# Optimization experiments

Hardware: AMD Instinct MI355X
Metric: run time of the kernel (lower is better)

## Reference

```python
import jax, jax.numpy as jnp
import numpy as np
from jax import lax

V, B, C_IN, T = 8, 32, 8, 4096
O, K, H = 64, 5, 16  # out_channels, kernel, SE hidden (O // reduction)
PAD = (K - 1) // 2


def setup_inputs() -> dict:
    key = jax.random.key(0)
    ks = jax.random.split(key, 8)
    return {
        "x": jax.random.normal(ks[0], (V, B, C_IN, T), dtype=jnp.float32),
        "conv_w": jax.random.uniform(ks[1], (O, 1, K), dtype=jnp.float32),
        "conv_b": jax.random.uniform(ks[2], (O,), dtype=jnp.float32),
        "se_w1": jax.random.normal(ks[3], (V, H, O), dtype=jnp.float32) * 0.1,
        "se_b1": jax.random.normal(ks[4], (V, H), dtype=jnp.float32) * 0.1,
        "se_w2": jax.random.normal(ks[5], (V, O, H), dtype=jnp.float32) * 0.1,
        "se_b2": jax.random.normal(ks[6], (V, O), dtype=jnp.float32) * 0.1,
        "attn_w": jax.random.normal(ks[7], (2 * O,), dtype=jnp.float32) * 0.1,
    }


def reference(x, conv_w, conv_b, se_w1, se_b1, se_w2, se_b2, attn_w):
    # _CommonConv1d: per-out-channel depthwise conv summed over input channels
    # == conv1d(sum over input channels) with weight [O,1,K].
    xs = x.sum(axis=2).reshape(V * B, 1, T)  # [V*B, 1, T]
    conv = lax.conv_general_dilated(
        xs, conv_w, window_strides=(1,), padding=[(PAD, PAD)],
        dimension_numbers=("NCH", "OIH", "NCH"))  # [V*B, O, T]
    conv = conv + conv_b[None, :, None]
    conv = jax.nn.selu(conv).reshape(V, B, O, T)  # conv_outputs, SELU activation

    # Per-vertex squeeze-excitation gating, then AdaptiveAvgPool1d(1)
    s = conv.mean(axis=-1)  # [V, B, O]
    h = jax.nn.relu(jnp.einsum("vbo,vho->vbh", s, se_w1) + se_b1[:, None, :])
    gate = jax.nn.sigmoid(jnp.einsum("vbh,voh->vbo", h, se_w2) + se_b2[:, None, :])
    compressed = (conv * gate[..., None]).mean(axis=-1)  # [V, B, O]

    # Pairwise self-attention over all (v_from, v_to) pairs
    cf = jnp.broadcast_to(compressed[:, None], (V, V, B, O))   # v_from
    ct = jnp.broadcast_to(compressed[None, :], (V, V, B, O))   # v_to
    feat = jnp.concatenate([cf, ct], axis=-1)                  # [Vf, Vt, B, 2O]
    aw = jax.nn.selu(jnp.einsum("fgbc,c->fgb", feat, attn_w))  # [Vf, Vt, B]
    sm = jax.nn.softmax(aw, axis=0)                            # softmax over v_from

    # outputs[v_to] = sum_f sm[f, v_to] * conv_outputs[f]
    out = jnp.einsum("fgb,fbot->gbot", sm, conv)  # [Vt, B, O, T]
    return out
```

## Files before the change

### kernel.cpp

```cpp
#include <hip/hip_runtime.h>

#define V 8
#define B 32
#define CIN 8
#define T 4096
#define O 64
#define K 5
#define H 16

#define XSTRIDE 4104

#define XS_OFF 0
#define S_OFF  (V*B*XSTRIDE)
#define AF_OFF (S_OFF + V*B*O)
#define AT_OFF (AF_OFF + V*B)
#define SM_OFF (AT_OFF + V*B)

__device__ __forceinline__ float selu_f(float x) {
    const float SC = 1.0507009873554805f;
    const float SA = 1.7580993408473766f;
    float e = __expf(x);
    float neg = SA * e - SA;
    return x > 0.0f ? SC * x : neg;
}

__global__ void k_xs(const float* __restrict__ x, float* __restrict__ ws) {
    int row = blockIdx.x;
    int tid = threadIdx.x;
    const float* xr = x + (size_t)row * CIN * T;
    float* xp = ws + XS_OFF + (size_t)row * XSTRIDE;
    for (int t = tid; t < T; t += 256) {
        float a = 0.0f;
        #pragma unroll
        for (int c = 0; c < CIN; ++c) a += xr[c * T + t];
        xp[t + 4] = a;
    }
    if (tid < 4) { xp[tid] = 0.0f; xp[4100 + tid] = 0.0f; }
}

__global__ void k_mean(const float* __restrict__ ws, const float* __restrict__ cw,
                       const float* __restrict__ cb, float* __restrict__ s_out) {
    int row = blockIdx.x;
    int tid = threadIdx.x;
    int wave = tid >> 6;
    int lane = tid & 63;
    const float* xp = ws + XS_OFF + (size_t)row * XSTRIDE;
    float w0 = cw[lane * 5 + 0], w1 = cw[lane * 5 + 1], w2 = cw[lane * 5 + 2];
    float w3 = cw[lane * 5 + 3], w4 = cw[lane * 5 + 4];
    float bv = cb[lane];
    int c0 = wave * 512;
    float a0 = xp[c0 + 2], a1 = xp[c0 + 3], a2 = xp[c0 + 4], a3 = xp[c0 + 5];
    float acc = 0.0f;
    #pragma unroll 8
    for (int t = c0; t < c0 + 512; ++t) {
        float a4 = xp[t + 6];
        float cv = bv + w0 * a0 + w1 * a1 + w2 * a2 + w3 * a3 + w4 * a4;
        acc += selu_f(cv);
        a0 = a1; a1 = a2; a2 = a3; a3 = a4;
    }
    __shared__ float part[8][64];
    part[wave][lane] = acc;
    __syncthreads();
    if (tid < 64) {
        float tot = 0.0f;
        #pragma unroll
        for (int w = 0; w < 8; ++w) tot += part[w][tid];
        s_out[row * 64 + tid] = tot * (1.0f / (float)T);
    }
}

__global__ void k_se(const float* __restrict__ s_in, const float* __restrict__ w1,
                     const float* __restrict__ b1, const float* __restrict__ w2,
                     const float* __restrict__ b2, const float* __restrict__ awv,
                     float* __restrict__ af, float* __restrict__ at) {
    int blk = blockIdx.x;
    int v = blk >> 5;
    int b = blk & 31;
    int o = threadIdx.x;
    __shared__ float ssh[64];
    __shared__ float hsh[16];
    float so = s_in[blk * 64 + o];
    ssh[o] = so;
    __syncthreads();
    if (o < 16) {
        float hv = b1[v * 16 + o];
        #pragma unroll
        for (int j = 0; j < 64; ++j) hv += ssh[j] * w1[(v * 16 + o) * 64 + j];
        hsh[o] = fmaxf(hv, 0.0f);
    }
    __syncthreads();
    float gv = b2[v * 64 + o];
    #pragma unroll
    for (int j = 0; j < 16; ++j) gv += hsh[j] * w2[(v * 64 + o) * 16 + j];
    float gate = 1.0f / (1.0f + __expf(-gv));
    float comp = so * gate;
    float pf = comp * awv[o];
    float pt = comp * awv[64 + o];
    #pragma unroll
    for (int m = 32; m >= 1; m >>= 1) {
        pf += __shfl_xor(pf, m, 64);
        pt += __shfl_xor(pt, m, 64);
    }
    if (o == 0) { af[v * 32 + b] = pf; at[v * 32 + b] = pt; }
}

__global__ void k_sm(const float* __restrict__ af, const float* __restrict__ at,
                     float* __restrict__ sm) {
    int b = blockIdx.x;
    int tid = threadIdx.x;
    int f = tid >> 3, g = tid & 7;
    float a = selu_f(af[f * 32 + b] + at[g * 32 + b]);
    float m = a;
    m = fmaxf(m, __shfl_xor(m, 8, 64));
    m = fmaxf(m, __shfl_xor(m, 16, 64));
    m = fmaxf(m, __shfl_xor(m, 32, 64));
    float e = __expf(a - m);
    float ssum = e;
    ssum += __shfl_xor(ssum, 8, 64);
    ssum += __shfl_xor(ssum, 16, 64);
    ssum += __shfl_xor(ssum, 32, 64);
    sm[b * 64 + tid] = e / ssum;
}

__global__ void k_out(const float* __restrict__ ws, const float* __restrict__ cw,
                      const float* __restrict__ cb, float* __restrict__ out) {
    int blk = blockIdx.x;
    int b = blk >> 6;
    int r = blk & 63;
    int tile = r >> 2;
    int og = r & 3;
    int t = tile * 256 + threadIdx.x;

    const float* smp = ws + SM_OFF + b * 64;
    float smv[64];
    #pragma unroll
    for (int i = 0; i < 64; ++i) smv[i] = smp[i];

    float xw[8][5];
    #pragma unroll
    for (int f = 0; f < 8; ++f) {
        const float* xp = ws + XS_OFF + (size_t)(f * B + b) * XSTRIDE + t + 2;
        #pragma unroll
        for (int j = 0; j < 5; ++j) xw[f][j] = xp[j];
    }

    #pragma unroll 1
    for (int oi = 0; oi < 16; ++oi) {
        int o = og * 16 + oi;
        float w0 = cw[o * 5 + 0], w1 = cw[o * 5 + 1], w2 = cw[o * 5 + 2];
        float w3 = cw[o * 5 + 3], w4 = cw[o * 5 + 4];
        float bv = cb[o];
        float cf[8];
        #pragma unroll
        for (int f = 0; f < 8; ++f) {
            float cv = bv + w0 * xw[f][0] + w1 * xw[f][1] + w2 * xw[f][2]
                          + w3 * xw[f][3] + w4 * xw[f][4];
            cf[f] = selu_f(cv);
        }
        #pragma unroll
        for (int g = 0; g < 8; ++g) {
            float acc = 0.0f;
            #pragma unroll
            for (int f = 0; f < 8; ++f) acc += smv[f * 8 + g] * cf[f];
            out[((size_t)(g * B + b) * O + o) * T + t] = acc;
        }
    }
}

extern "C" void kernel_launch(void* const* d_in, const int* in_sizes, int n_in,
                              void* d_out, int out_size, void* d_ws, size_t ws_size,
                              hipStream_t stream) {
    const float* x      = (const float*)d_in[0];
    const float* conv_w = (const float*)d_in[1];
    const float* conv_b = (const float*)d_in[2];
    const float* se_w1  = (const float*)d_in[3];
    const float* se_b1  = (const float*)d_in[4];
    const float* se_w2  = (const float*)d_in[5];
    const float* se_b2  = (const float*)d_in[6];
    const float* attn_w = (const float*)d_in[7];
    float* out = (float*)d_out;
    float* ws  = (float*)d_ws;

    k_xs<<<V * B, 256, 0, stream>>>(x, ws);
    k_mean<<<V * B, 512, 0, stream>>>(ws, conv_w, conv_b, ws + S_OFF);
    k_se<<<V * B, 64, 0, stream>>>(ws + S_OFF, se_w1, se_b1, se_w2, se_b2, attn_w,
                                   ws + AF_OFF, ws + AT_OFF);
    k_sm<<<B, 64, 0, stream>>>(ws + AF_OFF, ws + AT_OFF, ws + SM_OFF);
    k_out<<<B * (T / 256) * 4, 256, 0, stream>>>(ws, conv_w, conv_b, out);
}
```

Before: 113.0 us.

## Fuse prep kernels and vectorize output kernel with 4 timesteps per thread

Fuses the channel-sum kernel with the conv/SELU mean kernel, keeping the summed row in shared memory, and fuses the SE gating with the softmax kernel, which cuts five launches to three. The output kernel now computes four consecutive timesteps per thread from an 8-wide register window, writes float4 stores, and loads weights and softmax values through readfirstlane so they become uniform scalar values. The aim is less launch overhead, less global traffic and wider memory transactions. In exchange the output grid shrinks to 512 blocks, and the larger per-thread accumulator set raises register pressure and may reduce occupancy.

```diff
diff --git a/kernel.cpp b/kernel.cpp
--- a/kernel.cpp
+++ b/kernel.cpp
@@ -12,9 +12,7 @@
 
 #define XS_OFF 0
 #define S_OFF  (V*B*XSTRIDE)
-#define AF_OFF (S_OFF + V*B*O)
-#define AT_OFF (AF_OFF + V*B)
-#define SM_OFF (AT_OFF + V*B)
+#define SM_OFF (S_OFF + V*B*O)
 
 __device__ __forceinline__ float selu_f(float x) {
     const float SC = 1.0507009873554805f;
@@ -24,36 +22,53 @@
     return x > 0.0f ? SC * x : neg;
 }
 
-__global__ void k_xs(const float* __restrict__ x, float* __restrict__ ws) {
+__device__ __forceinline__ float sload(const float* p) {
+    return __int_as_float(__builtin_amdgcn_readfirstlane(__float_as_int(*p)));
+}
+
+__global__ __launch_bounds__(512) void k_xs_mean(
+        const float* __restrict__ x, const float* __restrict__ cw,
+        const float* __restrict__ cb, float* __restrict__ ws,
+        float* __restrict__ s_out) {
     int row = blockIdx.x;
     int tid = threadIdx.x;
+    __shared__ float xsh[XSTRIDE];
     const float* xr = x + (size_t)row * CIN * T;
     float* xp = ws + XS_OFF + (size_t)row * XSTRIDE;
-    for (int t = tid; t < T; t += 256) {
-        float a = 0.0f;
-        #pragma unroll
-        for (int c = 0; c < CIN; ++c) a += xr[c * T + t];
-        xp[t + 4] = a;
-    }
-    if (tid < 4) { xp[tid] = 0.0f; xp[4100 + tid] = 0.0f; }
-}
-
-__global__ void k_mean(const float* __restrict__ ws, const float* __restrict__ cw,
-                       const float* __restrict__ cb, float* __restrict__ s_out) {
-    int row = blockIdx.x;
-    int tid = threadIdx.x;
+
+    {
+        int t0 = tid * 8;
+        float4 a0 = make_float4(0.f, 0.f, 0.f, 0.f);
+        float4 a1 = make_float4(0.f, 0.f, 0.f, 0.f);
+        #pragma unroll
+        for (int c = 0; c < CIN; ++c) {
+            const float4* q = (const float4*)(xr + c * T + t0);
+            float4 u = q[0], v2 = q[1];
+            a0.x += u.x; a0.y += u.y; a0.z += u.z; a0.w += u.w;
+            a1.x += v2.x; a1.y += v2.y; a1.z += v2.z; a1.w += v2.w;
+        }
+        *(float4*)(&xsh[t0 + 4]) = a0;
+        *(float4*)(&xsh[t0 + 8]) = a1;
+        *(float4*)(xp + t0 + 4) = a0;
+        *(float4*)(xp + t0 + 8) = a1;
+        if (tid < 4) {
+            xsh[tid] = 0.0f; xsh[4100 + tid] = 0.0f;
+            xp[tid] = 0.0f;  xp[4100 + tid] = 0.0f;
+        }
+    }
+    __syncthreads();
+
     int wave = tid >> 6;
     int lane = tid & 63;
-    const float* xp = ws + XS_OFF + (size_t)row * XSTRIDE;
     float w0 = cw[lane * 5 + 0], w1 = cw[lane * 5 + 1], w2 = cw[lane * 5 + 2];
     float w3 = cw[lane * 5 + 3], w4 = cw[lane * 5 + 4];
     float bv = cb[lane];
     int c0 = wave * 512;
-    float a0 = xp[c0 + 2], a1 = xp[c0 + 3], a2 = xp[c0 + 4], a3 = xp[c0 + 5];
+    float a0 = xsh[c0 + 2], a1 = xsh[c0 + 3], a2 = xsh[c0 + 4], a3 = xsh[c0 + 5];
     float acc = 0.0f;
     #pragma unroll 8
     for (int t = c0; t < c0 + 512; ++t) {
-        float a4 = xp[t + 6];
+        float a4 = xsh[t + 6];
         float cv = bv + w0 * a0 + w1 * a1 + w2 * a2 + w3 * a3 + w4 * a4;
         acc += selu_f(cv);
         a0 = a1; a1 = a2; a2 = a3; a3 = a4;
@@ -69,29 +84,31 @@
     }
 }
 
-__global__ void k_se(const float* __restrict__ s_in, const float* __restrict__ w1,
-                     const float* __restrict__ b1, const float* __restrict__ w2,
-                     const float* __restrict__ b2, const float* __restrict__ awv,
-                     float* __restrict__ af, float* __restrict__ at) {
-    int blk = blockIdx.x;
-    int v = blk >> 5;
-    int b = blk & 31;
-    int o = threadIdx.x;
-    __shared__ float ssh[64];
-    __shared__ float hsh[16];
-    float so = s_in[blk * 64 + o];
-    ssh[o] = so;
+__global__ __launch_bounds__(512) void k_se_sm(
+        const float* __restrict__ s_in, const float* __restrict__ w1,
+        const float* __restrict__ b1, const float* __restrict__ w2,
+        const float* __restrict__ b2, const float* __restrict__ awv,
+        float* __restrict__ sm) {
+    int b = blockIdx.x;
+    int tid = threadIdx.x;
+    int v = tid >> 6;
+    int o = tid & 63;
+    __shared__ float ssh[8][64];
+    __shared__ float hsh[8][16];
+    __shared__ float afs[8], ats[8];
+    float so = s_in[(v * B + b) * 64 + o];
+    ssh[v][o] = so;
     __syncthreads();
     if (o < 16) {
         float hv = b1[v * 16 + o];
         #pragma unroll
-        for (int j = 0; j < 64; ++j) hv += ssh[j] * w1[(v * 16 + o) * 64 + j];
-        hsh[o] = fmaxf(hv, 0.0f);
+        for (int j = 0; j < 64; ++j) hv += ssh[v][j] * w1[(v * 16 + o) * 64 + j];
+        hsh[v][o] = fmaxf(hv, 0.0f);
     }
     __syncthreads();
     float gv = b2[v * 64 + o];
     #pragma unroll
-    for (int j = 0; j < 16; ++j) gv += hsh[j] * w2[(v * 64 + o) * 16 + j];
+    for (int j = 0; j < 16; ++j) gv += hsh[v][j] * w2[(v * 64 + o) * 16 + j];
     float gate = 1.0f / (1.0f + __expf(-gv));
     float comp = so * gate;
     float pf = comp * awv[o];
@@ -101,68 +118,83 @@
         pf += __shfl_xor(pf, m, 64);
         pt += __shfl_xor(pt, m, 64);
     }
-    if (o == 0) { af[v * 32 + b] = pf; at[v * 32 + b] = pt; }
-}
-
-__global__ void k_sm(const float* __restrict__ af, const float* __restrict__ at,
-                     float* __restrict__ sm) {
-    int b = blockIdx.x;
-    int tid = threadIdx.x;
-    int f = tid >> 3, g = tid & 7;
-    float a = selu_f(af[f * 32 + b] + at[g * 32 + b]);
-    float m = a;
-    m = fmaxf(m, __shfl_xor(m, 8, 64));
-    m = fmaxf(m, __shfl_xor(m, 16, 64));
-    m = fmaxf(m, __shfl_xor(m, 32, 64));
-    float e = __expf(a - m);
-    float ssum = e;
-    ssum += __shfl_xor(ssum, 8, 64);
-    ssum += __shfl_xor(ssum, 16, 64);
-    ssum += __shfl_xor(ssum, 32, 64);
-    sm[b * 64 + tid] = e / ssum;
-}
-
-__global__ void k_out(const float* __restrict__ ws, const float* __restrict__ cw,
-                      const float* __restrict__ cb, float* __restrict__ out) {
+    if (o == 0) { afs[v] = pf; ats[v] = pt; }
+    __syncthreads();
+    if (tid < 64) {
+        int f = tid >> 3, g = tid & 7;
+        float a = selu_f(afs[f] + ats[g]);
+        float m = a;
+        m = fmaxf(m, __shfl_xor(m, 8, 64));
+        m = fmaxf(m, __shfl_xor(m, 16, 64));
+        m = fmaxf(m, __shfl_xor(m, 32, 64));
+        float e = __expf(a - m);
+        float ssum = e;
+        ssum += __shfl_xor(ssum, 8, 64);
+        ssum += __shfl_xor(ssum, 16, 64);
+        ssum += __shfl_xor(ssum, 32, 64);
+        sm[b * 64 + tid] = e / ssum;
+    }
+}
+
+__global__ __launch_bounds__(256) void k_out(
+        const float* __restrict__ ws, const float* __restrict__ cw,
+        const float* __restrict__ cb, float* __restrict__ out) {
     int blk = blockIdx.x;
-    int b = blk >> 6;
-    int r = blk & 63;
+    int b = blk >> 4;
+    int r = blk & 15;
     int tile = r >> 2;
     int og = r & 3;
-    int t = tile * 256 + threadIdx.x;
+    int t0 = tile * 1024 + threadIdx.x * 4;
 
     const float* smp = ws + SM_OFF + b * 64;
     float smv[64];
     #pragma unroll
-    for (int i = 0; i < 64; ++i) smv[i] = smp[i];
-
-    float xw[8][5];
+    for (int i = 0; i < 64; ++i) smv[i] = sload(smp + i);
+
+    float xw[8][8];
     #pragma unroll
     for (int f = 0; f < 8; ++f) {
-        const float* xp = ws + XS_OFF + (size_t)(f * B + b) * XSTRIDE + t + 2;
-        #pragma unroll
-        for (int j = 0; j < 5; ++j) xw[f][j] = xp[j];
+        const float* xp = ws + XS_OFF + (size_t)(f * B + b) * XSTRIDE + t0;
+        float4 q0 = *(const float4*)(xp);
+        float4 q1 = *(const float4*)(xp + 4);
+        float4 q2 = *(const float4*)(xp + 8);
+        xw[f][0] = q0.z; xw[f][1] = q0.w;
+        xw[f][2] = q1.x; xw[f][3] = q1.y; xw[f][4] = q1.z; xw[f][5] = q1.w;
+        xw[f][6] = q2.x; xw[f][7] = q2.y;
     }
 
     #pragma unroll 1
     for (int oi = 0; oi < 16; ++oi) {
         int o = og * 16 + oi;
-        float w0 = cw[o * 5 + 0], w1 = cw[o * 5 + 1], w2 = cw[o * 5 + 2];
-        float w3 = cw[o * 5 + 3], w4 = cw[o * 5 + 4];
-        float bv = cb[o];
-        float cf[8];
+        float w0 = sload(cw + o * 5 + 0), w1 = sload(cw + o * 5 + 1);
+        float w2 = sload(cw + o * 5 + 2), w3 = sload(cw + o * 5 + 3);
+        float w4 = sload(cw + o * 5 + 4);
+        float bv = sload(cb + o);
+        float acc[8][4];
+        #pragma unroll
+        for (int g = 0; g < 8; ++g)
+            #pragma unroll
+            for (int dt = 0; dt < 4; ++dt) acc[g][dt] = 0.0f;
         #pragma unroll
         for (int f = 0; f < 8; ++f) {
-            float cv = bv + w0 * xw[f][0] + w1 * xw[f][1] + w2 * xw[f][2]
-                          + w3 * xw[f][3] + w4 * xw[f][4];
-            cf[f] = selu_f(cv);
+            float cv[4];
+            #pragma unroll
+            for (int dt = 0; dt < 4; ++dt) {
+                float c = bv + w0 * xw[f][dt] + w1 * xw[f][dt + 1] + w2 * xw[f][dt + 2]
+                             + w3 * xw[f][dt + 3] + w4 * xw[f][dt + 4];
+                cv[dt] = selu_f(c);
+            }
+            #pragma unroll
+            for (int g = 0; g < 8; ++g) {
+                float s = smv[f * 8 + g];
+                #pragma unroll
+                for (int dt = 0; dt < 4; ++dt) acc[g][dt] += s * cv[dt];
+            }
         }
         #pragma unroll
         for (int g = 0; g < 8; ++g) {
-            float acc = 0.0f;
-            #pragma unroll
-            for (int f = 0; f < 8; ++f) acc += smv[f * 8 + g] * cf[f];
-            out[((size_t)(g * B + b) * O + o) * T + t] = acc;
+            float4 o4 = make_float4(acc[g][0], acc[g][1], acc[g][2], acc[g][3]);
+            *(float4*)(out + ((size_t)(g * B + b) * O + o) * T + t0) = o4;
         }
     }
 }
@@ -181,10 +213,8 @@
     float* out = (float*)d_out;
     float* ws  = (float*)d_ws;
 
-    k_xs<<<V * B, 256, 0, stream>>>(x, ws);
-    k_mean<<<V * B, 512, 0, stream>>>(ws, conv_w, conv_b, ws + S_OFF);
-    k_se<<<V * B, 64, 0, stream>>>(ws + S_OFF, se_w1, se_b1, se_w2, se_b2, attn_w,
-                                   ws + AF_OFF, ws + AT_OFF);
-    k_sm<<<B, 64, 0, stream>>>(ws + AF_OFF, ws + AT_OFF, ws + SM_OFF);
-    k_out<<<B * (T / 256) * 4, 256, 0, stream>>>(ws, conv_w, conv_b, out);
-}
+    k_xs_mean<<<V * B, 512, 0, stream>>>(x, conv_w, conv_b, ws, ws + S_OFF);
+    k_se_sm<<<B, 512, 0, stream>>>(ws + S_OFF, se_w1, se_b1, se_w2, se_b2, attn_w,
+                                   ws + SM_OFF);
+    k_out<<<B * 4 * 4, 256, 0, stream>>>(ws, conv_w, conv_b, out);
+}
```

After: 107.4 us. -5.0%, faster.
